# Kernel optimization log

Hardware: AMD Instinct MI355X
Metric: run time of the kernel (lower is better)

The kernel has to match this reference:

```python
import jax, jax.numpy as jnp
import numpy as np

N = 50000       # nodes
E = 800000      # raw edges (self-loops added in reference, per PyG GATConv default)
F_IN = 256      # input feature dim (dataset.num_features stand-in)
H = 4           # heads (layer 1)
C = 32          # hidden_channels per head
CLS = 16        # num_classes (layer 2 out, heads=1)


def setup_inputs() -> dict:
    key = jax.random.key(0)
    ks = jax.random.split(key, 12)
    s = 0.05
    return {
        "x": jax.random.normal(ks[0], (N, F_IN), jnp.float32),
        "edge_index": jax.random.randint(ks[1], (2, E), 0, N, dtype=jnp.int64),
        "W1": jax.random.normal(ks[2], (F_IN, H * C), jnp.float32) * s,
        "att_src1": jax.random.normal(ks[3], (H, C), jnp.float32) * s,
        "att_dst1": jax.random.normal(ks[4], (H, C), jnp.float32) * s,
        "b1": jnp.zeros((H * C,), jnp.float32),
        "W2": jax.random.normal(ks[5], (H * C, CLS), jnp.float32) * s,
        "att_src2": jax.random.normal(ks[6], (1, CLS), jnp.float32) * s,
        "att_dst2": jax.random.normal(ks[7], (1, CLS), jnp.float32) * s,
        "b2": jnp.zeros((CLS,), jnp.float32),
    }


def gat_conv(x, src, dst, W, a_src, a_dst, b, heads, ch):
    """One GATConv (concat=True). src/dst include self-loops."""
    n = x.shape[0]
    h = (x @ W).reshape(n, heads, ch)                       # [N,H,C]
    alpha_s = jnp.sum(h * a_src, axis=-1)                   # [N,H]
    alpha_d = jnp.sum(h * a_dst, axis=-1)                   # [N,H]
    e = jax.nn.leaky_relu(alpha_s[src] + alpha_d[dst], 0.2) # [E',H]
    # segment softmax over incoming edges of each destination node
    m = jax.ops.segment_max(e, dst, num_segments=n)         # [N,H]
    ex = jnp.exp(e - m[dst])
    den = jax.ops.segment_sum(ex, dst, num_segments=n)      # [N,H]
    coef = ex / (den[dst] + 1e-16)                          # [E',H]
    # weighted scatter-aggregate of source features
    out = jax.ops.segment_sum(h[src] * coef[:, :, None], dst, num_segments=n)
    return out.reshape(n, heads * ch) + b


def reference(x, edge_index, W1, att_src1, att_dst1, b1, W2, att_src2, att_dst2, b2):
    n = x.shape[0]
    loop = jnp.arange(n, dtype=edge_index.dtype)
    src = jnp.concatenate([edge_index[0], loop])
    dst = jnp.concatenate([edge_index[1], loop])
    # eval mode: F.dropout is identity
    h = gat_conv(x, src, dst, W1, att_src1, att_dst1, b1, H, C)
    h = jax.nn.elu(h)
    out = gat_conv(h, src, dst, W2, att_src2, att_dst2, b2, 1, CLS)
    return out
```

## Files before the change

kernel.cpp:

```cpp
#include <hip/hip_runtime.h>
#include <hip/hip_bf16.h>
#include <math.h>

#define NNODES 50000
#define FIN 256
#define HH 4
#define CC 32
#define D1 128
#define CLS 16
#define NBUCK ((NNODES + 255) >> 8)
#define CHUNK 4096

typedef __attribute__((ext_vector_type(8))) short bfrag8;
typedef __attribute__((ext_vector_type(4))) float facc4;

__device__ __forceinline__ float lrelu(float x){ return x > 0.f ? x : 0.2f*x; }

__device__ __forceinline__ float fexp(float x){
#if __has_builtin(__builtin_amdgcn_exp2f)
  return __builtin_amdgcn_exp2f(x * 1.4426950408889634f);
#else
  return exp2f(x * 1.4426950408889634f);
#endif
}

__device__ __forceinline__ unsigned short f2bu(float x){
  __hip_bfloat16 h = __float2bfloat16(x);
  return *reinterpret_cast<unsigned short*>(&h);
}
__device__ __forceinline__ unsigned int pbf(float a, float b){
  return (unsigned int)f2bu(a) | ((unsigned int)f2bu(b) << 16);
}
__device__ __forceinline__ float2 bf2x(unsigned int u){
  float2 r;
  r.x = __uint_as_float(u << 16);
  r.y = __uint_as_float(u & 0xffff0000u);
  return r;
}

__global__ void wprep_kernel(const float* __restrict__ W, unsigned short* __restrict__ Wt) {
  int t = blockIdx.x*256 + threadIdx.x;
  if (t >= FIN*D1) return;
  int k = t >> 7, c = t & 127;
  Wt[c*FIN + k] = f2bu(W[t]);
}

__global__ __launch_bounds__(256) void gemm1_mfma(const float* __restrict__ x,
                                                  const unsigned int* __restrict__ Wt,
                                                  const float* __restrict__ asrc,
                                                  const float* __restrict__ adst,
                                                  unsigned int* __restrict__ h1b,
                                                  float* __restrict__ as1,
                                                  float* __restrict__ ad1) {
  __shared__ unsigned int Bs[128*256/2];
  __shared__ unsigned int As[64*64/2];
  int tid = threadIdx.x;
  int wv = tid >> 6, lane = tid & 63;
  int r0 = blockIdx.x * 64;

  for (int it = 0; it < 16; it++) {
    int w16 = it*256 + tid;
    int c = w16 >> 5, k8 = w16 & 31;
    uint4 v = ((const uint4*)Wt)[w16];
    int byt = (c*512 + k8*16) ^ ((c&7)<<4);
    *(uint4*)((char*)Bs + byt) = v;
  }

  facc4 acc[8];
  #pragma unroll
  for (int t=0;t<8;t++) acc[t] = (facc4){0.f,0.f,0.f,0.f};

  int arow = tid >> 2, apart = tid & 3;
  int mrow = lane & 15, kb = lane >> 4;

  for (int stage = 0; stage < 4; stage++) {
    int gr = r0 + arow;
    const float* src = x + (size_t)gr*FIN + stage*64 + apart*16;
    float4 f0, f1, f2, f3;
    if (gr < NNODES) {
      f0 = *(const float4*)(src);
      f1 = *(const float4*)(src+4);
      f2 = *(const float4*)(src+8);
      f3 = *(const float4*)(src+12);
    } else {
      f0 = f1 = f2 = f3 = make_float4(0.f,0.f,0.f,0.f);
    }
    uint4 u0, u1;
    u0.x = pbf(f0.x,f0.y); u0.y = pbf(f0.z,f0.w);
    u0.z = pbf(f1.x,f1.y); u0.w = pbf(f1.z,f1.w);
    u1.x = pbf(f2.x,f2.y); u1.y = pbf(f2.z,f2.w);
    u1.z = pbf(f3.x,f3.y); u1.w = pbf(f3.z,f3.w);
    __syncthreads();
    int b0 = (arow*128 + apart*32) ^ ((arow&7)<<4);
    int b1 = (arow*128 + apart*32 + 16) ^ ((arow&7)<<4);
    *(uint4*)((char*)As + b0) = u0;
    *(uint4*)((char*)As + b1) = u1;
    __syncthreads();
    #pragma unroll
    for (int ks = 0; ks < 2; ks++) {
      int row = wv*16 + mrow;
      int abyt = (row*128 + ks*64 + kb*16) ^ ((row&7)<<4);
      bfrag8 afrag = *(bfrag8*)((char*)As + abyt);
      #pragma unroll
      for (int ct = 0; ct < 8; ct++) {
        int c = ct*16 + mrow;
        int bbyt = (c*512 + stage*128 + ks*64 + kb*16) ^ ((c&7)<<4);
        bfrag8 bfrag = *(bfrag8*)((char*)Bs + bbyt);
        acc[ct] = __builtin_amdgcn_mfma_f32_16x16x32_bf16(afrag, bfrag, acc[ct], 0, 0, 0);
      }
    }
  }
  int orow0 = r0 + wv*16 + (lane>>4)*4;
  int ocol = lane & 15;
  float asr[8], adr[8];
  #pragma unroll
  for (int ct=0; ct<8; ct++){
    asr[ct] = asrc[ct*16 + ocol];
    adr[ct] = adst[ct*16 + ocol];
  }
  #pragma unroll
  for (int r=0; r<4; r++) {
    int gr = orow0 + r;
    float sh[4], dh[4];
    #pragma unroll
    for (int h=0; h<4; h++){
      sh[h] = acc[2*h][r]*asr[2*h] + acc[2*h+1][r]*asr[2*h+1];
      dh[h] = acc[2*h][r]*adr[2*h] + acc[2*h+1][r]*adr[2*h+1];
    }
    #pragma unroll
    for (int off=1; off<16; off<<=1){
      #pragma unroll
      for (int h=0;h<4;h++){
        sh[h] += __shfl_xor(sh[h], off, 64);
        dh[h] += __shfl_xor(dh[h], off, 64);
      }
    }
    if (gr < NNODES) {
      if (ocol == 0) {
        *(float4*)(as1 + (size_t)gr*4) = make_float4(sh[0], sh[1], sh[2], sh[3]);
        *(float4*)(ad1 + (size_t)gr*4) = make_float4(dh[0], dh[1], dh[2], dh[3]);
      }
      #pragma unroll
      for (int ct=0; ct<4; ct++)
        h1b[(size_t)gr*64 + ct*16 + ocol] = pbf(acc[ct][r], acc[ct+4][r]);
    }
  }
}

__global__ __launch_bounds__(256) void bucket_count_kernel(const int* __restrict__ dsts,
                                                           int* __restrict__ bcnt, int E) {
  __shared__ int cnt[NBUCK];
  for (int t=threadIdx.x; t<NBUCK; t+=256) cnt[t]=0;
  __syncthreads();
  int base = blockIdx.x*CHUNK, lim = min(base+CHUNK, E);
  for (int e = base+threadIdx.x; e < lim; e += 256)
    atomicAdd(&cnt[dsts[e]>>8], 1);
  __syncthreads();
  for (int t=threadIdx.x; t<NBUCK; t+=256)
    if (cnt[t]) atomicAdd(&bcnt[t], cnt[t]);
}

__global__ __launch_bounds__(256) void bucket_scan_kernel(const int* __restrict__ bcnt,
                                                          int* __restrict__ gstart,
                                                          int* __restrict__ gcur) {
  int t = threadIdx.x;
  int orig = (t < NBUCK) ? bcnt[t] : 0;
  int v = orig;
  int ln = t & 63, wv = t >> 6;
  #pragma unroll
  for (int off=1; off<64; off<<=1){ int u=__shfl_up(v,off,64); if(ln>=off) v+=u; }
  __shared__ int wsum[4], wbase[4];
  if (ln==63) wsum[wv]=v;
  __syncthreads();
  if (t==0){
    int s=0;
    for(int k=0;k<4;k++){ wbase[k]=s; s+=wsum[k]; }
  }
  __syncthreads();
  int incl = wbase[wv]+v;
  if (t < NBUCK){ gstart[t+1]=incl; gcur[t]=incl-orig; }
  if (t==0) gstart[0]=0;
}

__global__ __launch_bounds__(256) void bin_kernel(const int* __restrict__ srcs,
                                                  const int* __restrict__ dsts,
                                                  int* __restrict__ gcur,
                                                  unsigned int* __restrict__ binned, int E) {
  __shared__ int cnt[NBUCK];
  __shared__ int rbase[NBUCK];
  for (int t=threadIdx.x; t<NBUCK; t+=256) cnt[t]=0;
  __syncthreads();
  int base = blockIdx.x*CHUNK, lim = min(base+CHUNK, E);
  for (int e = base+threadIdx.x; e < lim; e += 256)
    atomicAdd(&cnt[dsts[e]>>8], 1);
  __syncthreads();
  for (int t=threadIdx.x; t<NBUCK; t+=256){
    rbase[t] = cnt[t] ? atomicAdd(&gcur[t], cnt[t]) : 0;
    cnt[t] = 0;
  }
  __syncthreads();
  for (int e = base+threadIdx.x; e < lim; e += 256){
    int d = dsts[e], s = srcs[e];
    int b = d >> 8;
    int p = rbase[b] + atomicAdd(&cnt[b], 1);
    binned[p] = ((unsigned int)s << 8) | (unsigned int)(d & 255);
  }
}

__global__ __launch_bounds__(256) void bucketcsr_kernel(const int* __restrict__ gstart,
                                                        const unsigned int* __restrict__ binned,
                                                        int* __restrict__ offs,
                                                        unsigned short* __restrict__ srcsort, int E) {
  int b = blockIdx.x;
  int s0 = gstart[b], s1 = gstart[b+1];
  int t = threadIdx.x;
  __shared__ int cnt[256];
  __shared__ int cur[256];
  cnt[t] = 0;
  __syncthreads();
  for (int j = s0+t; j < s1; j += 256)
    atomicAdd(&cnt[binned[j] & 255], 1);
  __syncthreads();
  int orig = cnt[t], v = orig;
  int ln = t & 63, wv = t >> 6;
  #pragma unroll
  for (int off=1; off<64; off<<=1){ int u=__shfl_up(v,off,64); if(ln>=off) v+=u; }
  __shared__ int wsum[4], wbase[4];
  if (ln==63) wsum[wv]=v;
  __syncthreads();
  if (t==0){
    int s=0;
    for(int k=0;k<4;k++){ wbase[k]=s; s+=wsum[k]; }
  }
  __syncthreads();
  int excl = wbase[wv] + v - orig;
  cur[t] = excl;
  int node = b*256 + t;
  if (node < NNODES) offs[node] = s0 + excl;
  if (node == NNODES-1) offs[NNODES] = E;
  __syncthreads();
  for (int j = s0+t; j < s1; j += 256){
    unsigned int e = binned[j];
    int p = s0 + atomicAdd(&cur[e & 255], 1);
    srcsort[p] = (unsigned short)(e >> 8);
  }
}

__global__ __launch_bounds__(256) void agg1_kernel(
    const unsigned int* __restrict__ h1b, const float* __restrict__ as1,
    const float* __restrict__ ad1, const int* __restrict__ offs,
    const unsigned short* __restrict__ srcsort, const float* __restrict__ b1,
    unsigned int* __restrict__ out1p) {
  __shared__ float exs[4][4][64];
  __shared__ int   ss [4][64];
  int warp = threadIdx.x >> 6;
  int lane = threadIdx.x & 63;
  int i = blockIdx.x * 4 + warp;
  if (i >= NNODES) return;
  int start = offs[i], end = offs[i+1];
  float4 adv = *(const float4*)(ad1 + (size_t)i*4);
  float4 asv = *(const float4*)(as1 + (size_t)i*4);
  float ad[4] = {adv.x, adv.y, adv.z, adv.w};
  float wself[4];
  {
    float av[4] = {asv.x, asv.y, asv.z, asv.w};
    #pragma unroll
    for (int h=0;h<4;h++) wself[h] = fexp(lrelu(av[h] + ad[h]));
  }
  int hlo = lane >> 5, hhi = hlo + 2;
  float den[4] = {0.f, 0.f, 0.f, 0.f};
  float accA, accB;
  {
    float2 hv = bf2x(h1b[(size_t)i*64 + lane]);
    accA = wself[hlo] * hv.x; accB = wself[hhi] * hv.y;
  }
  for (int c0 = start; c0 < end; c0 += 64) {
    int cnt = min(64, end - c0);
    int j = c0 + lane;
    if (j < end) {
      int s = (int)srcsort[j];
      float4 a = *(const float4*)(as1 + (size_t)s*4);
      float e0 = fexp(lrelu(a.x + ad[0]));
      float e1 = fexp(lrelu(a.y + ad[1]));
      float e2 = fexp(lrelu(a.z + ad[2]));
      float e3 = fexp(lrelu(a.w + ad[3]));
      den[0] += e0; den[1] += e1; den[2] += e2; den[3] += e3;
      exs[warp][0][lane] = e0; exs[warp][1][lane] = e1;
      exs[warp][2][lane] = e2; exs[warp][3][lane] = e3;
      ss[warp][lane] = s;
    }
    #pragma unroll 8
    for (int j2 = 0; j2 < cnt; j2++) {
      int s = ss[warp][j2];
      float2 hv = bf2x(h1b[(size_t)s*64 + lane]);
      accA = fmaf(exs[warp][hlo][j2], hv.x, accA);
      accB = fmaf(exs[warp][hhi][j2], hv.y, accB);
    }
  }
  #pragma unroll
  for (int off=1; off<64; off<<=1) {
    #pragma unroll
    for (int h=0;h<4;h++) den[h] += __shfl_xor(den[h], off, 64);
  }
  float invlo = 1.f / (den[hlo] + wself[hlo] + 1e-16f);
  float invhi = 1.f / (den[hhi] + wself[hhi] + 1e-16f);
  float v0 = accA * invlo + b1[lane];
  float v1 = accB * invhi + b1[lane + 64];
  v0 = v0 > 0.f ? v0 : fexp(v0) - 1.f;
  v1 = v1 > 0.f ? v1 : fexp(v1) - 1.f;
  out1p[(size_t)i*64 + lane] = pbf(v0, v1);
}

__global__ __launch_bounds__(256) void layer2_proj_kernel(
    const unsigned int* __restrict__ out1p, const float* __restrict__ W2,
    const float* __restrict__ asrc2, const float* __restrict__ adst2,
    __hip_bfloat16* __restrict__ h2b, float* __restrict__ as2, float* __restrict__ ad2) {
  __shared__ float w_s[D1*CLS];
  for (int l = threadIdx.x; l < D1*CLS; l += 256) w_s[l] = W2[l];
  __syncthreads();
  int warp = threadIdx.x >> 6, lane = threadIdx.x & 63;
  int i = blockIdx.x*4 + warp;
  if (i >= NNODES) return;
  int c = lane & 15, kq = lane >> 4;
  const unsigned int* xp = out1p + (size_t)i*64 + (kq&1)*32;
  bool hi = kq >= 2;
  int kb = (kq&1)*32 + (hi ? 64 : 0);
  float acc = 0.f;
  #pragma unroll
  for (int q8=0; q8<8; q8++) {
    uint4 u = *(const uint4*)(xp + q8*4);
    float v0 = hi ? bf2x(u.x).y : bf2x(u.x).x;
    float v1 = hi ? bf2x(u.y).y : bf2x(u.y).x;
    float v2 = hi ? bf2x(u.z).y : bf2x(u.z).x;
    float v3 = hi ? bf2x(u.w).y : bf2x(u.w).x;
    int k = kb + q8*4;
    acc = fmaf(v0, w_s[(k+0)*CLS + c], acc);
    acc = fmaf(v1, w_s[(k+1)*CLS + c], acc);
    acc = fmaf(v2, w_s[(k+2)*CLS + c], acc);
    acc = fmaf(v3, w_s[(k+3)*CLS + c], acc);
  }
  acc += __shfl_xor(acc, 16, 64);
  acc += __shfl_xor(acc, 32, 64);
  if (lane < 16) h2b[(size_t)i*CLS + c] = __float2bfloat16(acc);
  float s = acc * asrc2[c];
  float d = acc * adst2[c];
  #pragma unroll
  for (int off=1; off<16; off<<=1) { s += __shfl_xor(s, off, 64); d += __shfl_xor(d, off, 64); }
  if (lane == 0) { as2[i] = s; ad2[i] = d; }
}

__global__ __launch_bounds__(256) void agg2_kernel(
    const unsigned int* __restrict__ h2b, const float* __restrict__ as2,
    const float* __restrict__ ad2, const int* __restrict__ offs,
    const unsigned short* __restrict__ srcsort, const float* __restrict__ b2,
    float* __restrict__ out) {
  int warp = threadIdx.x >> 6, lane = threadIdx.x & 63;
  int i = blockIdx.x*4 + warp;
  if (i >= NNODES) return;
  int start = offs[i], end = offs[i+1];
  float ad = ad2[i];
  float wself = fexp(lrelu(as2[i] + ad));
  int g = lane >> 3, cp = lane & 7;
  float2 acc = make_float2(0.f, 0.f);
  float denp = 0.f;
  if (g == 0) {
    float2 hv = bf2x(h2b[(size_t)i*(CLS/2) + cp]);
    acc.x = wself*hv.x; acc.y = wself*hv.y;
    denp = wself;
  }
  #pragma unroll 4
  for (int j = start + g; j < end; j += 8) {
    int s = (int)srcsort[j];
    float w = fexp(lrelu(as2[s] + ad));
    denp += w;
    float2 hv = bf2x(h2b[(size_t)s*(CLS/2) + cp]);
    acc.x = fmaf(w, hv.x, acc.x);
    acc.y = fmaf(w, hv.y, acc.y);
  }
  #pragma unroll
  for (int off=8; off<64; off<<=1) {
    acc.x += __shfl_xor(acc.x, off, 64);
    acc.y += __shfl_xor(acc.y, off, 64);
    denp  += __shfl_xor(denp,  off, 64);
  }
  if (lane < 8) {
    float inv = 1.f / (denp + 1e-16f);
    float2 o;
    o.x = acc.x * inv + b2[2*cp];
    o.y = acc.y * inv + b2[2*cp+1];
    *(float2*)(out + (size_t)i*CLS + 2*cp) = o;
  }
}

extern "C" void kernel_launch(void* const* d_in, const int* in_sizes, int n_in,
                              void* d_out, int out_size, void* d_ws, size_t ws_size,
                              hipStream_t stream) {
  const float* x     = (const float*)d_in[0];
  const int*   eidx  = (const int*)d_in[1];
  const float* W1    = (const float*)d_in[2];
  const float* asrc1 = (const float*)d_in[3];
  const float* adst1 = (const float*)d_in[4];
  const float* b1    = (const float*)d_in[5];
  const float* W2    = (const float*)d_in[6];
  const float* asrc2 = (const float*)d_in[7];
  const float* adst2 = (const float*)d_in[8];
  const float* b2    = (const float*)d_in[9];
  float* out = (float*)d_out;

  const int E = in_sizes[1] / 2;
  const int* srcs = eidx;
  const int* dsts = eidx + E;
  const int EBLK = (E + CHUNK - 1) / CHUNK;

  char* ws = (char*)d_ws;
  size_t off = 0;
  auto alloc = [&](size_t bytes) -> void* {
    void* p = ws + off;
    off = (off + bytes + 255) & ~(size_t)255;
    return p;
  };
  unsigned int*   h1b     = (unsigned int*)alloc((size_t)NNODES*(D1/2)*4);
  unsigned int*   out1p   = (unsigned int*)alloc((size_t)NNODES*(D1/2)*4);
  unsigned short* Wt      = (unsigned short*)alloc((size_t)FIN*D1*2);
  float*          as1     = (float*)alloc((size_t)NNODES*HH*4);
  float*          ad1     = (float*)alloc((size_t)NNODES*HH*4);
  __hip_bfloat16* h2b     = (__hip_bfloat16*)alloc((size_t)NNODES*CLS*2);
  float*          as2     = (float*)alloc((size_t)NNODES*4);
  float*          ad2     = (float*)alloc((size_t)NNODES*4);
  int*            bcnt    = (int*)alloc((size_t)NBUCK*4);
  int*            gstart  = (int*)alloc((size_t)(NBUCK+1)*4);
  int*            gcur    = (int*)alloc((size_t)NBUCK*4);
  int*            offs    = (int*)alloc((size_t)(NNODES+1)*4);
  unsigned int*   binned  = (unsigned int*)alloc((size_t)E*4);
  unsigned short* srcsort = (unsigned short*)alloc((size_t)E*2);

  (void)hipMemsetAsync(bcnt, 0, (size_t)NBUCK*4, stream);

  wprep_kernel<<<(FIN*D1+255)/256, 256, 0, stream>>>(W1, Wt);
  gemm1_mfma<<<(NNODES+63)/64, 256, 0, stream>>>(x, (const unsigned int*)Wt,
                                                 asrc1, adst1, h1b, as1, ad1);

  bucket_count_kernel<<<EBLK, 256, 0, stream>>>(dsts, bcnt, E);
  bucket_scan_kernel<<<1, 256, 0, stream>>>(bcnt, gstart, gcur);
  bin_kernel<<<EBLK, 256, 0, stream>>>(srcs, dsts, gcur, binned, E);
  bucketcsr_kernel<<<NBUCK, 256, 0, stream>>>(gstart, binned, offs, srcsort, E);

  agg1_kernel<<<(NNODES+3)/4, 256, 0, stream>>>(h1b, as1, ad1, offs, srcsort, b1, out1p);

  layer2_proj_kernel<<<(NNODES+3)/4, 256, 0, stream>>>(out1p, W2, asrc2, adst2, h2b, as2, ad2);
  agg2_kernel<<<(NNODES+3)/4, 256, 0, stream>>>((const unsigned int*)h2b, as2, ad2, offs, srcsort, b2, out);
}
```

Measured before the change: 153.0 us.

## Widen CSR build blocks, shrink count chunks, and stage agg2 edge weights in LDS

```diff
diff --git a/kernel.cpp b/kernel.cpp
--- a/kernel.cpp
+++ b/kernel.cpp
@@ -10,6 +10,7 @@
 #define CLS 16
 #define NBUCK ((NNODES + 255) >> 8)
 #define CHUNK 4096
+#define CHUNKC 1024
 
 typedef __attribute__((ext_vector_type(8))) short bfrag8;
 typedef __attribute__((ext_vector_type(4))) float facc4;
@@ -152,7 +153,7 @@
   __shared__ int cnt[NBUCK];
   for (int t=threadIdx.x; t<NBUCK; t+=256) cnt[t]=0;
   __syncthreads();
-  int base = blockIdx.x*CHUNK, lim = min(base+CHUNK, E);
+  int base = blockIdx.x*CHUNKC, lim = min(base+CHUNKC, E);
   for (int e = base+threadIdx.x; e < lim; e += 256)
     atomicAdd(&cnt[dsts[e]>>8], 1);
   __syncthreads();
@@ -182,24 +183,24 @@
   if (t==0) gstart[0]=0;
 }
 
-__global__ __launch_bounds__(256) void bin_kernel(const int* __restrict__ srcs,
-                                                  const int* __restrict__ dsts,
-                                                  int* __restrict__ gcur,
-                                                  unsigned int* __restrict__ binned, int E) {
+__global__ __launch_bounds__(1024) void bin_kernel(const int* __restrict__ srcs,
+                                                   const int* __restrict__ dsts,
+                                                   int* __restrict__ gcur,
+                                                   unsigned int* __restrict__ binned, int E) {
   __shared__ int cnt[NBUCK];
   __shared__ int rbase[NBUCK];
-  for (int t=threadIdx.x; t<NBUCK; t+=256) cnt[t]=0;
+  for (int t=threadIdx.x; t<NBUCK; t+=1024) cnt[t]=0;
   __syncthreads();
   int base = blockIdx.x*CHUNK, lim = min(base+CHUNK, E);
-  for (int e = base+threadIdx.x; e < lim; e += 256)
+  for (int e = base+threadIdx.x; e < lim; e += 1024)
     atomicAdd(&cnt[dsts[e]>>8], 1);
   __syncthreads();
-  for (int t=threadIdx.x; t<NBUCK; t+=256){
+  for (int t=threadIdx.x; t<NBUCK; t+=1024){
     rbase[t] = cnt[t] ? atomicAdd(&gcur[t], cnt[t]) : 0;
     cnt[t] = 0;
   }
   __syncthreads();
-  for (int e = base+threadIdx.x; e < lim; e += 256){
+  for (int e = base+threadIdx.x; e < lim; e += 1024){
     int d = dsts[e], s = srcs[e];
     int b = d >> 8;
     int p = rbase[b] + atomicAdd(&cnt[b], 1);
@@ -207,39 +208,44 @@
   }
 }
 
-__global__ __launch_bounds__(256) void bucketcsr_kernel(const int* __restrict__ gstart,
-                                                        const unsigned int* __restrict__ binned,
-                                                        int* __restrict__ offs,
-                                                        unsigned short* __restrict__ srcsort, int E) {
+__global__ __launch_bounds__(1024) void bucketcsr_kernel(const int* __restrict__ gstart,
+                                                         const unsigned int* __restrict__ binned,
+                                                         int* __restrict__ offs,
+                                                         unsigned short* __restrict__ srcsort, int E) {
   int b = blockIdx.x;
   int s0 = gstart[b], s1 = gstart[b+1];
   int t = threadIdx.x;
   __shared__ int cnt[256];
   __shared__ int cur[256];
-  cnt[t] = 0;
-  __syncthreads();
-  for (int j = s0+t; j < s1; j += 256)
+  __shared__ int wsum[4], wbase[4];
+  if (t < 256) cnt[t] = 0;
+  __syncthreads();
+  for (int j = s0+t; j < s1; j += 1024)
     atomicAdd(&cnt[binned[j] & 255], 1);
   __syncthreads();
-  int orig = cnt[t], v = orig;
+  int orig = 0, v = 0;
   int ln = t & 63, wv = t >> 6;
-  #pragma unroll
-  for (int off=1; off<64; off<<=1){ int u=__shfl_up(v,off,64); if(ln>=off) v+=u; }
-  __shared__ int wsum[4], wbase[4];
-  if (ln==63) wsum[wv]=v;
+  if (t < 256) {
+    orig = cnt[t]; v = orig;
+    #pragma unroll
+    for (int off=1; off<64; off<<=1){ int u=__shfl_up(v,off,64); if(ln>=off) v+=u; }
+    if (ln==63) wsum[wv]=v;
+  }
   __syncthreads();
   if (t==0){
     int s=0;
     for(int k=0;k<4;k++){ wbase[k]=s; s+=wsum[k]; }
   }
   __syncthreads();
-  int excl = wbase[wv] + v - orig;
-  cur[t] = excl;
-  int node = b*256 + t;
-  if (node < NNODES) offs[node] = s0 + excl;
-  if (node == NNODES-1) offs[NNODES] = E;
-  __syncthreads();
-  for (int j = s0+t; j < s1; j += 256){
+  if (t < 256) {
+    int excl = wbase[wv] + v - orig;
+    cur[t] = excl;
+    int node = b*256 + t;
+    if (node < NNODES) offs[node] = s0 + excl;
+    if (node == NNODES-1) offs[NNODES] = E;
+  }
+  __syncthreads();
+  for (int j = s0+t; j < s1; j += 1024){
     unsigned int e = binned[j];
     int p = s0 + atomicAdd(&cur[e & 255], 1);
     srcsort[p] = (unsigned short)(e >> 8);
@@ -354,6 +360,8 @@
     const float* __restrict__ ad2, const int* __restrict__ offs,
     const unsigned short* __restrict__ srcsort, const float* __restrict__ b2,
     float* __restrict__ out) {
+  __shared__ float wls[4][64];
+  __shared__ int   ss2[4][64];
   int warp = threadIdx.x >> 6, lane = threadIdx.x & 63;
   int i = blockIdx.x*4 + warp;
   if (i >= NNODES) return;
@@ -362,28 +370,38 @@
   float wself = fexp(lrelu(as2[i] + ad));
   int g = lane >> 3, cp = lane & 7;
   float2 acc = make_float2(0.f, 0.f);
-  float denp = 0.f;
+  float denp = (lane == 0) ? wself : 0.f;
   if (g == 0) {
     float2 hv = bf2x(h2b[(size_t)i*(CLS/2) + cp]);
     acc.x = wself*hv.x; acc.y = wself*hv.y;
-    denp = wself;
-  }
-  #pragma unroll 4
-  for (int j = start + g; j < end; j += 8) {
-    int s = (int)srcsort[j];
-    float w = fexp(lrelu(as2[s] + ad));
-    denp += w;
-    float2 hv = bf2x(h2b[(size_t)s*(CLS/2) + cp]);
-    acc.x = fmaf(w, hv.x, acc.x);
-    acc.y = fmaf(w, hv.y, acc.y);
+  }
+  for (int c0 = start; c0 < end; c0 += 64) {
+    int cnt = min(64, end - c0);
+    int j = c0 + lane;
+    if (j < end) {
+      int s = (int)srcsort[j];
+      float w = fexp(lrelu(as2[s] + ad));
+      denp += w;
+      wls[warp][lane] = w;
+      ss2[warp][lane] = s;
+    }
+    #pragma unroll 8
+    for (int j2 = g; j2 < cnt; j2 += 8) {
+      int s = ss2[warp][j2];
+      float w = wls[warp][j2];
+      float2 hv = bf2x(h2b[(size_t)s*(CLS/2) + cp]);
+      acc.x = fmaf(w, hv.x, acc.x);
+      acc.y = fmaf(w, hv.y, acc.y);
+    }
   }
   #pragma unroll
   for (int off=8; off<64; off<<=1) {
     acc.x += __shfl_xor(acc.x, off, 64);
     acc.y += __shfl_xor(acc.y, off, 64);
-    denp  += __shfl_xor(denp,  off, 64);
-  }
-  if (lane < 8) {
+  }
+  #pragma unroll
+  for (int off=1; off<64; off<<=1) denp += __shfl_xor(denp, off, 64);
+  if (g == 0) {
     float inv = 1.f / (denp + 1e-16f);
     float2 o;
     o.x = acc.x * inv + b2[2*cp];
@@ -410,7 +428,8 @@
   const int E = in_sizes[1] / 2;
   const int* srcs = eidx;
   const int* dsts = eidx + E;
-  const int EBLK = (E + CHUNK - 1) / CHUNK;
+  const int EBLK  = (E + CHUNK - 1) / CHUNK;
+  const int EBLKC = (E + CHUNKC - 1) / CHUNKC;
 
   char* ws = (char*)d_ws;
   size_t off = 0;
@@ -440,10 +459,10 @@
   gemm1_mfma<<<(NNODES+63)/64, 256, 0, stream>>>(x, (const unsigned int*)Wt,
                                                  asrc1, adst1, h1b, as1, ad1);
 
-  bucket_count_kernel<<<EBLK, 256, 0, stream>>>(dsts, bcnt, E);
+  bucket_count_kernel<<<EBLKC, 256, 0, stream>>>(dsts, bcnt, E);
   bucket_scan_kernel<<<1, 256, 0, stream>>>(bcnt, gstart, gcur);
-  bin_kernel<<<EBLK, 256, 0, stream>>>(srcs, dsts, gcur, binned, E);
-  bucketcsr_kernel<<<NBUCK, 256, 0, stream>>>(gstart, binned, offs, srcsort, E);
+  bin_kernel<<<EBLK, 1024, 0, stream>>>(srcs, dsts, gcur, binned, E);
+  bucketcsr_kernel<<<NBUCK, 1024, 0, stream>>>(gstart, binned, offs, srcsort, E);
 
   agg1_kernel<<<(NNODES+3)/4, 256, 0, stream>>>(h1b, as1, ad1, offs, srcsort, b1, out1p);
 
```

After: 156.9 us. 1.03x slower.
